# Kernel tuning notes

Hardware: AMD Instinct MI355X
Metric: run time of the kernel (lower is better)

## Reference

```python
import jax, jax.numpy as jnp
import numpy as np

NEG = -100.0
M2M, M2I, M2D, I2M, I2I, D2M, D2D = range(7)
LOG_Q = float(np.log(0.25))


def _d_chain(fM, aM2D, aD2D):
    """Sequential delete-state recurrence along motif axis k.
    fD[k] = logaddexp(aM2D[k-1] + fM[k-1], aD2D[k-1] + fD[k-1]), fD[0] = NEG.
    fM: (B, K+1); aM2D, aD2D: (B, K+1). Returns (B, K+1)."""
    B, Kp1 = fM.shape
    K = Kp1 - 1

    def step(fd_prev, inp):
        am, ad, fm = inp  # each (B,)
        fd = jnp.logaddexp(am + fm, ad + fd_prev)
        return fd, fd

    init = jnp.full((B,), NEG, dtype=fM.dtype)
    _, fds = jax.lax.scan(step, init, (aM2D[:, :K].T, aD2D[:, :K].T, fM[:, :K].T))
    return jnp.concatenate([init[:, None], fds.T], axis=1)


def _profile_hmm_loss(a, e, x):
    """pHMM forward algorithm (log-space). a: (B,K+1,7), e: (B,K,4), x: (B,L) int.
    Returns -log P(x) per batch element, shape (B,)."""
    B, Kp1, _ = a.shape
    K = Kp1 - 1

    fM0 = jnp.full((B, Kp1), NEG, dtype=a.dtype).at[:, 0].set(0.0)
    fI0 = jnp.full((B, Kp1), NEG, dtype=a.dtype)
    fD0 = _d_chain(fM0, a[:, :, M2D], a[:, :, D2D])

    def l_step(carry, x_l):
        fM, fI, fD = carry
        # emission for symbol x_l at each match state k: (B, K)
        esel = jnp.take_along_axis(e, x_l[:, None, None].astype(jnp.int32), axis=2)[:, :, 0]
        prev = jnp.logaddexp(
            jnp.logaddexp(a[:, :K, M2M] + fM[:, :K], a[:, :K, I2M] + fI[:, :K]),
            a[:, :K, D2M] + fD[:, :K],
        )
        fM_new = jnp.concatenate([jnp.full((B, 1), NEG, dtype=a.dtype), esel + prev], axis=1)
        fI_new = LOG_Q + jnp.logaddexp(a[:, :, M2I] + fM, a[:, :, I2I] + fI)
        fD_new = _d_chain(fM_new, a[:, :, M2D], a[:, :, D2D])
        return (fM_new, fI_new, fD_new), None

    (fM, fI, fD), _ = jax.lax.scan(l_step, (fM0, fI0, fD0), x.T)

    final = jnp.stack(
        [fM[:, K] + a[:, K, M2M], fI[:, K] + a[:, K, I2M], fD[:, K] + a[:, K, D2M]],
        axis=1,
    )
    return -jax.nn.logsumexp(final, axis=1)


def _kld_loss(mus, logvars):
    return -0.5 * jnp.sum(1.0 + logvars - mus * mus - jnp.exp(logvars), axis=1)


def setup_inputs() -> dict:
    key = jax.random.key(0)
    k1, k2, k3, k4, k5 = jax.random.split(key, 5)
    B, K, L, E = 4096, 64, 128, 16
    batch_input = jax.random.randint(k1, (B, L), 0, 4, dtype=jnp.int32)
    transition_probs = jax.random.normal(k2, (B, K + 1, 7), dtype=jnp.float32)
    emission_probs = jax.random.normal(k3, (B, K, 4), dtype=jnp.float32)
    mus = jax.random.normal(k4, (B, E), dtype=jnp.float32)
    logvars = jax.random.normal(k5, (B, E), dtype=jnp.float32)
    return {
        "batch_input": batch_input,
        "transition_probs": transition_probs,
        "emission_probs": emission_probs,
        "mus": mus,
        "logvars": logvars,
    }


def reference(batch_input, transition_probs, emission_probs, mus, logvars):
    beta = 1.0
    recon = jnp.mean(_profile_hmm_loss(transition_probs, emission_probs, batch_input))
    kld = jnp.mean(_kld_loss(mus, logvars))
    return recon + beta * kld
```

## Files before the change

### kernel.cpp

```cpp
#include <hip/hip_runtime.h>
#include <math.h>


namespace {

constexpr float kLog2e = 1.4426950408889634f;
constexpr float kLn2   = 0.6931471805599453f;

__device__ __forceinline__ float fexp(float x) {
    return __builtin_amdgcn_exp2f(x * kLog2e);
}

__device__ __forceinline__ float rflf(float x) {
    return __builtin_bit_cast(float,
        __builtin_amdgcn_readfirstlane(__builtin_bit_cast(int, x)));
}

template <int CTRL, bool BC>
__device__ __forceinline__ float dppf(float old, float src) {
    int r = __builtin_amdgcn_update_dpp(__builtin_bit_cast(int, old),
                                        __builtin_bit_cast(int, src),
                                        CTRL, 0xF, 0xF, BC);
    return __builtin_bit_cast(float, r);
}

__global__ __launch_bounds__(256) void phmm_vae_kernel(
    const int* __restrict__ xg,
    const float* __restrict__ ag,
    const float* __restrict__ eg,
    const float* __restrict__ mug,
    const float* __restrict__ lvg,
    float* __restrict__ out, int B)
{
    const int tid  = threadIdx.x;
    const int lane = tid & 63;
    const int wv   = tid >> 6;
    const int b    = (blockIdx.x << 2) + wv;

    __shared__ float part[4];
    float contrib = 0.0f;

    if (b < B) {
        const float* ab = ag + (size_t)b * 455;
        const float* eb = eg + (size_t)b * 256;
        const int*   xb = xg + (size_t)b * 128;

        const int j = lane;
        const float a2 = ab[j * 7 + 2];
        const float a6 = ab[j * 7 + 6];
        const float a5 = ab[(j + 1) * 7 + 5];
        const float A1M2M  = fexp(ab[(j + 1) * 7 + 0]);
        const float QA1M2I = 0.25f * fexp(ab[(j + 1) * 7 + 1]);
        const float A1I2M  = fexp(ab[(j + 1) * 7 + 3]);
        const float QA1I2I = 0.25f * fexp(ab[(j + 1) * 7 + 4]);
        const float A0M2M = fexp(ab[0]);
        const float D0f = rflf(0.25f * fexp(ab[4]));
        const float G0f = rflf(0.25f * fexp(ab[3] + ab[1] - ab[0]));

        float4 ev = *reinterpret_cast<const float4*>(eb + j * 4);
        const float E0 = fexp(ev.x), E1 = fexp(ev.y);
        const float E2 = fexp(ev.z), E3 = fexp(ev.w);

        const int xlo = xb[lane];
        const int xhi = xb[64 + lane];
        const unsigned long long b0lo = __ballot(xlo & 1);
        const unsigned long long b1lo = __ballot(xlo & 2);
        const unsigned long long b0hi = __ballot(xhi & 1);
        const unsigned long long b1hi = __ballot(xhi & 2);

        const float a5p = dppf<0x138, false>(0.0f, a5);
        const float dh  = fexp(a6 + a5 - a5p);
        const float wM2D = fexp(a2 + a5);
        const float Cf0 = wM2D * dppf<0x138, false>(0.0f, E0);
        const float Cf1 = wM2D * dppf<0x138, false>(0.0f, E1);
        const float Cf2 = wM2D * dppf<0x138, false>(0.0f, E2);
        const float Cf3 = wM2D * dppf<0x138, false>(0.0f, E3);

        auto bfr = [](float x) -> unsigned {
            unsigned u = __builtin_bit_cast(unsigned, x);
            return (u + 0x8000u) >> 16;
        };
        const int E10 = (int)((bfr(E1) << 16) | bfr(E0));
        const int E32 = (int)((bfr(E3) << 16) | bfr(E2));
        const int C10 = (int)((bfr(Cf1) << 16) | bfr(Cf0));
        const int C32 = (int)((bfr(Cf3) << 16) | bfr(Cf2));

        const float V1 = dh;
        const float V2 = V1 * dppf<0x111, false>(1.0f, V1);
        const float V4 = V2 * dppf<0x112, false>(1.0f, V2);
        const float V8 = V4 * dppf<0x114, false>(1.0f, V4);
        const float V1m = (lane >= 1)  ? V1 : 0.0f;
        const float V2m = (lane >= 2)  ? V2 : 0.0f;
        const float V4m = (lane >= 4)  ? V4 : 0.0f;
        const float V8m = (lane >= 8)  ? V8 : 0.0f;
        float Q = dh;
        Q *= dppf<0x111, false>(1.0f, Q);
        Q *= dppf<0x112, false>(1.0f, Q);
        Q *= dppf<0x114, false>(1.0f, Q);
        Q *= dppf<0x118, false>(1.0f, Q);
        const int   row = lane >> 4;
        const float Q47 = __shfl(Q, 47, 64);
        const float QmA = (row == 1 || row == 3) ? Q : 0.0f;
        const float QmB = (row == 2) ? Q : ((row == 3) ? Q * Q47 : 0.0f);

        float y0 = (lane == 0) ? wM2D : 0.0f;
        y0 = fmaf(V1m, dppf<0x111, true>(0.0f, y0), y0);
        y0 = fmaf(V2m, dppf<0x112, true>(0.0f, y0), y0);
        y0 = fmaf(V4m, dppf<0x114, true>(0.0f, y0), y0);
        y0 = fmaf(V8m, dppf<0x118, true>(0.0f, y0), y0);
        y0 = fmaf(QmA, dppf<0x142, true>(0.0f, y0), y0);
        y0 = fmaf(QmB, dppf<0x143, true>(0.0f, y0), y0);

        auto sel_of = [&](int l) -> int {
            const unsigned long long m0 = (l & 64) ? b0hi : b0lo;
            const unsigned long long m1 = (l & 64) ? b1hi : b1lo;
            const int sh = l & 63;
            unsigned s = (unsigned)((m0 >> sh) & 1ull) |
                         ((unsigned)((m1 >> sh) & 1ull) << 1);
            return (int)(0x00000C0Cu + s * 0x02020000u + 0x01000000u);
        };

        float fM = 0.0f, fI = 0.0f;
        float pl = y0;
        float p0 = A0M2M;
        float LS = 0.0f;

        const int sel0 = sel_of(0);
        float E = __builtin_bit_cast(float,
            __builtin_amdgcn_perm((unsigned)E32, (unsigned)E10, (unsigned)sel0));
        float C = __builtin_bit_cast(float,
            __builtin_amdgcn_perm((unsigned)C32, (unsigned)C10, (unsigned)sel0));

#pragma unroll 8
        for (int l = 0; l < 128; ++l) {
            const int seln = sel_of((l + 1) & 127);
            const float mul_s = (l == 0) ? G0f : D0f;

            float y, pv, En, Cn;
            asm("v_mul_f32 %[fI], %[QI2I], %[fI]\n\t"
                "v_mov_b32 %[pv], %[p0]\n\t"
                "v_perm_b32 %[En], %[e32], %[e10], %[sel]\n\t"
                "v_perm_b32 %[Cn], %[c32], %[c10], %[sel]\n\t"
                "v_mov_b32_dpp %[pv], %[pl] wave_shr:1 row_mask:0xf bank_mask:0xf\n\t"
                "v_fmac_f32 %[fI], %[QM2I], %[fM]\n\t"
                "v_mul_f32 %[p0], %[mul], %[p0]\n\t"
                "v_mul_f32_dpp %[y], %[pv], %[C] wave_shr:1 row_mask:0xf bank_mask:0xf bound_ctrl:0\n\t"
                "v_mul_f32 %[fM], %[E], %[pv]\n\t"
                "s_nop 0\n\t"
                "v_fmac_f32_dpp %[y], %[y], %[V1] row_shr:1 row_mask:0xf bank_mask:0xf bound_ctrl:0\n\t"
                "s_nop 1\n\t"
                "v_fmac_f32_dpp %[y], %[y], %[V2] row_shr:2 row_mask:0xf bank_mask:0xf bound_ctrl:0\n\t"
                "s_nop 1\n\t"
                "v_fmac_f32_dpp %[y], %[y], %[V4] row_shr:4 row_mask:0xf bank_mask:0xf bound_ctrl:0\n\t"
                "s_nop 1\n\t"
                "v_fmac_f32_dpp %[y], %[y], %[V8] row_shr:8 row_mask:0xf bank_mask:0xf bound_ctrl:0\n\t"
                "s_nop 1\n\t"
                "v_fmac_f32_dpp %[y], %[y], %[QmA] row_bcast:15 row_mask:0xf bank_mask:0xf bound_ctrl:0\n\t"
                "s_nop 1\n\t"
                "v_fmac_f32_dpp %[y], %[y], %[QmB] row_bcast:31 row_mask:0xf bank_mask:0xf bound_ctrl:0\n\t"
                "v_fmac_f32 %[y], %[I2M], %[fI]\n\t"
                "v_fmac_f32 %[y], %[M2M], %[fM]"
                : [y] "=&v"(y), [pv] "=&v"(pv), [En] "=&v"(En), [Cn] "=&v"(Cn),
                  [fM] "+v"(fM), [fI] "+v"(fI), [p0] "+v"(p0)
                : [pl] "v"(pl), [E] "v"(E), [C] "v"(C),
                  [e32] "v"(E32), [e10] "v"(E10),
                  [c32] "v"(C32), [c10] "v"(C10),
                  [V1] "v"(V1m), [V2] "v"(V2m), [V4] "v"(V4m), [V8] "v"(V8m),
                  [QmA] "v"(QmA), [QmB] "v"(QmB),
                  [QI2I] "v"(QA1I2I), [QM2I] "v"(QA1M2I),
                  [I2M] "v"(A1I2M), [M2M] "v"(A1M2M),
                  [sel] "s"(seln), [mul] "s"(mul_s));
            pl = y;
            E = En;
            C = Cn;

            if ((l & 15) == 15) {
                float m = fmaxf(fmaxf(fM, fI), pl);
                m = fmaxf(m, dppf<0xB1,  true>(0.0f, m));
                m = fmaxf(m, dppf<0x4E,  true>(0.0f, m));
                m = fmaxf(m, dppf<0x141, true>(0.0f, m));
                m = fmaxf(m, dppf<0x140, true>(0.0f, m));
                m = fmaxf(m, 1e-35f);
                int mb = __builtin_bit_cast(int, m);
                unsigned u0 = (unsigned)__builtin_amdgcn_readlane(mb, 0);
                unsigned u1 = (unsigned)__builtin_amdgcn_readlane(mb, 16);
                unsigned u2 = (unsigned)__builtin_amdgcn_readlane(mb, 32);
                unsigned u3 = (unsigned)__builtin_amdgcn_readlane(mb, 48);
                unsigned ua = u0 > u1 ? u0 : u1;
                unsigned ub = u2 > u3 ? u2 : u3;
                unsigned um = ua > ub ? ua : ub;
                int ee = (int)(um >> 23);
                float r = __builtin_bit_cast(float, (unsigned)(254 - ee) << 23);
                LS += (float)(ee - 127);
                fM *= r; fI *= r; pl *= r; p0 *= r;
            }
        }

        const float Fv = __shfl(pl, 63, 64);
        const float loss = -(__builtin_amdgcn_logf(Fv) + LS) * kLn2;

        float kt = 0.0f;
        if (lane < 16) {
            float mu = mug[(size_t)b * 16 + lane];
            float lv = lvg[(size_t)b * 16 + lane];
            kt = 1.0f + lv - mu * mu - fexp(lv);
        }
        kt += __shfl_xor(kt, 1, 64);
        kt += __shfl_xor(kt, 2, 64);
        kt += __shfl_xor(kt, 4, 64);
        kt += __shfl_xor(kt, 8, 64);
        float kldb = __shfl(-0.5f * kt, 0, 64);

        contrib = (loss + kldb) * (1.0f / 4096.0f);
    }

    if (lane == 63) part[wv] = (b < B) ? contrib : 0.0f;
    __syncthreads();
    if (tid == 0) {
        atomicAdd(out, part[0] + part[1] + part[2] + part[3]);
    }
}

}

extern "C" void kernel_launch(void* const* d_in, const int* in_sizes, int n_in,
                              void* d_out, int out_size, void* d_ws, size_t ws_size,
                              hipStream_t stream) {
    const int*   x  = (const int*)d_in[0];
    const float* a  = (const float*)d_in[1];
    const float* e  = (const float*)d_in[2];
    const float* mu = (const float*)d_in[3];
    const float* lv = (const float*)d_in[4];
    float* out = (float*)d_out;

    const int B = in_sizes[0] / 128;
    const int grid = (B + 3) / 4;

    phmm_vae_kernel<<<grid, 256, 0, stream>>>(x, a, e, mu, lv, out, B);
}
```

Before: 92.28 us.

## Process two batch elements per wave with interleaved DPP recurrence chains

Each wavefront now runs the forward recurrence for two sequences at once, interleaving their DPP scan instructions so each chain's dependent DPP ops fill the other's stall slots instead of explicit s_nop padding. The grid is halved accordingly, and the KLD term is computed for both elements using lanes 0-31. This roughly doubles per-wave register use and halves the number of waves, which may reduce latency hiding from occupancy; some inline-asm work moved to compiler-scheduled C++.

```diff
diff --git a/kernel.cpp b/kernel.cpp
--- a/kernel.cpp
+++ b/kernel.cpp
@@ -22,6 +22,125 @@
                                         __builtin_bit_cast(int, src),
                                         CTRL, 0xF, 0xF, BC);
     return __builtin_bit_cast(float, r);
+}
+
+__device__ __forceinline__ unsigned bfr(float x) {
+    unsigned u = __builtin_bit_cast(unsigned, x);
+    return (u + 0x8000u) >> 16;
+}
+
+struct Elem {
+    float fM, fI, pl, p0, E, C, LS;
+    float V1m, V2m, V4m, V8m, QmA, QmB;
+    float QI2I, QM2I, I2M, M2M;
+    float D0, G0;
+    int E10, E32, C10, C32;
+    unsigned long long b0lo, b1lo, b0hi, b1hi;
+};
+
+__device__ __forceinline__ int sel_of(const Elem& s, int l) {
+    const unsigned long long m0 = (l & 64) ? s.b0hi : s.b0lo;
+    const unsigned long long m1 = (l & 64) ? s.b1hi : s.b1lo;
+    const int sh = l & 63;
+    unsigned t = (unsigned)((m0 >> sh) & 1ull) |
+                 ((unsigned)((m1 >> sh) & 1ull) << 1);
+    return (int)(0x00000C0Cu + t * 0x02020000u + 0x01000000u);
+}
+
+__device__ __forceinline__ void setup(Elem& s, const float* __restrict__ ab,
+                                      const float* __restrict__ eb,
+                                      const int* __restrict__ xb, int lane) {
+    const int j = lane;
+    const float a2 = ab[j * 7 + 2];
+    const float a6 = ab[j * 7 + 6];
+    const float a5 = ab[(j + 1) * 7 + 5];
+    s.M2M  = fexp(ab[(j + 1) * 7 + 0]);
+    s.QM2I = 0.25f * fexp(ab[(j + 1) * 7 + 1]);
+    s.I2M  = fexp(ab[(j + 1) * 7 + 3]);
+    s.QI2I = 0.25f * fexp(ab[(j + 1) * 7 + 4]);
+    const float A0M2M = fexp(ab[0]);
+    s.D0 = rflf(0.25f * fexp(ab[4]));
+    s.G0 = rflf(0.25f * fexp(ab[3] + ab[1] - ab[0]));
+
+    float4 ev = *reinterpret_cast<const float4*>(eb + j * 4);
+    const float E0 = fexp(ev.x), E1 = fexp(ev.y);
+    const float E2 = fexp(ev.z), E3 = fexp(ev.w);
+
+    const int xlo = xb[lane];
+    const int xhi = xb[64 + lane];
+    s.b0lo = __ballot(xlo & 1);
+    s.b1lo = __ballot(xlo & 2);
+    s.b0hi = __ballot(xhi & 1);
+    s.b1hi = __ballot(xhi & 2);
+
+    const float a5p = dppf<0x138, false>(0.0f, a5);
+    const float dh  = fexp(a6 + a5 - a5p);
+    const float wM2D = fexp(a2 + a5);
+    const float Cf0 = wM2D * dppf<0x138, false>(0.0f, E0);
+    const float Cf1 = wM2D * dppf<0x138, false>(0.0f, E1);
+    const float Cf2 = wM2D * dppf<0x138, false>(0.0f, E2);
+    const float Cf3 = wM2D * dppf<0x138, false>(0.0f, E3);
+
+    s.E10 = (int)((bfr(E1) << 16) | bfr(E0));
+    s.E32 = (int)((bfr(E3) << 16) | bfr(E2));
+    s.C10 = (int)((bfr(Cf1) << 16) | bfr(Cf0));
+    s.C32 = (int)((bfr(Cf3) << 16) | bfr(Cf2));
+
+    const float V1 = dh;
+    const float V2 = V1 * dppf<0x111, false>(1.0f, V1);
+    const float V4 = V2 * dppf<0x112, false>(1.0f, V2);
+    const float V8 = V4 * dppf<0x114, false>(1.0f, V4);
+    s.V1m = (lane >= 1) ? V1 : 0.0f;
+    s.V2m = (lane >= 2) ? V2 : 0.0f;
+    s.V4m = (lane >= 4) ? V4 : 0.0f;
+    s.V8m = (lane >= 8) ? V8 : 0.0f;
+    float Q = dh;
+    Q *= dppf<0x111, false>(1.0f, Q);
+    Q *= dppf<0x112, false>(1.0f, Q);
+    Q *= dppf<0x114, false>(1.0f, Q);
+    Q *= dppf<0x118, false>(1.0f, Q);
+    const int   row = lane >> 4;
+    const float Q47 = __shfl(Q, 47, 64);
+    s.QmA = (row == 1 || row == 3) ? Q : 0.0f;
+    s.QmB = (row == 2) ? Q : ((row == 3) ? Q * Q47 : 0.0f);
+
+    float y0 = (lane == 0) ? wM2D : 0.0f;
+    y0 = fmaf(s.V1m, dppf<0x111, true>(0.0f, y0), y0);
+    y0 = fmaf(s.V2m, dppf<0x112, true>(0.0f, y0), y0);
+    y0 = fmaf(s.V4m, dppf<0x114, true>(0.0f, y0), y0);
+    y0 = fmaf(s.V8m, dppf<0x118, true>(0.0f, y0), y0);
+    y0 = fmaf(s.QmA, dppf<0x142, true>(0.0f, y0), y0);
+    y0 = fmaf(s.QmB, dppf<0x143, true>(0.0f, y0), y0);
+
+    s.fM = 0.0f; s.fI = 0.0f; s.LS = 0.0f;
+    s.pl = y0;
+    s.p0 = A0M2M;
+    const int sel0 = sel_of(s, 0);
+    s.E = __builtin_bit_cast(float,
+        __builtin_amdgcn_perm((unsigned)s.E32, (unsigned)s.E10, (unsigned)sel0));
+    s.C = __builtin_bit_cast(float,
+        __builtin_amdgcn_perm((unsigned)s.C32, (unsigned)s.C10, (unsigned)sel0));
+}
+
+__device__ __forceinline__ void rescale(Elem& s) {
+    float m = fmaxf(fmaxf(s.fM, s.fI), s.pl);
+    m = fmaxf(m, dppf<0xB1,  true>(0.0f, m));
+    m = fmaxf(m, dppf<0x4E,  true>(0.0f, m));
+    m = fmaxf(m, dppf<0x141, true>(0.0f, m));
+    m = fmaxf(m, dppf<0x140, true>(0.0f, m));
+    m = fmaxf(m, 1e-35f);
+    int mb = __builtin_bit_cast(int, m);
+    unsigned u0 = (unsigned)__builtin_amdgcn_readlane(mb, 0);
+    unsigned u1 = (unsigned)__builtin_amdgcn_readlane(mb, 16);
+    unsigned u2 = (unsigned)__builtin_amdgcn_readlane(mb, 32);
+    unsigned u3 = (unsigned)__builtin_amdgcn_readlane(mb, 48);
+    unsigned ua = u0 > u1 ? u0 : u1;
+    unsigned ub = u2 > u3 ? u2 : u3;
+    unsigned um = ua > ub ? ua : ub;
+    int ee = (int)(um >> 23);
+    float r = __builtin_bit_cast(float, (unsigned)(254 - ee) << 23);
+    s.LS += (float)(ee - 127);
+    s.fM *= r; s.fI *= r; s.pl *= r; s.p0 *= r;
 }
 
 __global__ __launch_bounds__(256) void phmm_vae_kernel(
@@ -35,186 +154,112 @@
     const int tid  = threadIdx.x;
     const int lane = tid & 63;
     const int wv   = tid >> 6;
-    const int b    = (blockIdx.x << 2) + wv;
+    const int pr   = (blockIdx.x << 2) + wv;
+    const int bA   = pr << 1;
+    const int bBr  = bA + 1;
 
     __shared__ float part[4];
     float contrib = 0.0f;
 
-    if (b < B) {
-        const float* ab = ag + (size_t)b * 455;
-        const float* eb = eg + (size_t)b * 256;
-        const int*   xb = xg + (size_t)b * 128;
-
-        const int j = lane;
-        const float a2 = ab[j * 7 + 2];
-        const float a6 = ab[j * 7 + 6];
-        const float a5 = ab[(j + 1) * 7 + 5];
-        const float A1M2M  = fexp(ab[(j + 1) * 7 + 0]);
-        const float QA1M2I = 0.25f * fexp(ab[(j + 1) * 7 + 1]);
-        const float A1I2M  = fexp(ab[(j + 1) * 7 + 3]);
-        const float QA1I2I = 0.25f * fexp(ab[(j + 1) * 7 + 4]);
-        const float A0M2M = fexp(ab[0]);
-        const float D0f = rflf(0.25f * fexp(ab[4]));
-        const float G0f = rflf(0.25f * fexp(ab[3] + ab[1] - ab[0]));
-
-        float4 ev = *reinterpret_cast<const float4*>(eb + j * 4);
-        const float E0 = fexp(ev.x), E1 = fexp(ev.y);
-        const float E2 = fexp(ev.z), E3 = fexp(ev.w);
-
-        const int xlo = xb[lane];
-        const int xhi = xb[64 + lane];
-        const unsigned long long b0lo = __ballot(xlo & 1);
-        const unsigned long long b1lo = __ballot(xlo & 2);
-        const unsigned long long b0hi = __ballot(xhi & 1);
-        const unsigned long long b1hi = __ballot(xhi & 2);
-
-        const float a5p = dppf<0x138, false>(0.0f, a5);
-        const float dh  = fexp(a6 + a5 - a5p);
-        const float wM2D = fexp(a2 + a5);
-        const float Cf0 = wM2D * dppf<0x138, false>(0.0f, E0);
-        const float Cf1 = wM2D * dppf<0x138, false>(0.0f, E1);
-        const float Cf2 = wM2D * dppf<0x138, false>(0.0f, E2);
-        const float Cf3 = wM2D * dppf<0x138, false>(0.0f, E3);
-
-        auto bfr = [](float x) -> unsigned {
-            unsigned u = __builtin_bit_cast(unsigned, x);
-            return (u + 0x8000u) >> 16;
-        };
-        const int E10 = (int)((bfr(E1) << 16) | bfr(E0));
-        const int E32 = (int)((bfr(E3) << 16) | bfr(E2));
-        const int C10 = (int)((bfr(Cf1) << 16) | bfr(Cf0));
-        const int C32 = (int)((bfr(Cf3) << 16) | bfr(Cf2));
-
-        const float V1 = dh;
-        const float V2 = V1 * dppf<0x111, false>(1.0f, V1);
-        const float V4 = V2 * dppf<0x112, false>(1.0f, V2);
-        const float V8 = V4 * dppf<0x114, false>(1.0f, V4);
-        const float V1m = (lane >= 1)  ? V1 : 0.0f;
-        const float V2m = (lane >= 2)  ? V2 : 0.0f;
-        const float V4m = (lane >= 4)  ? V4 : 0.0f;
-        const float V8m = (lane >= 8)  ? V8 : 0.0f;
-        float Q = dh;
-        Q *= dppf<0x111, false>(1.0f, Q);
-        Q *= dppf<0x112, false>(1.0f, Q);
-        Q *= dppf<0x114, false>(1.0f, Q);
-        Q *= dppf<0x118, false>(1.0f, Q);
-        const int   row = lane >> 4;
-        const float Q47 = __shfl(Q, 47, 64);
-        const float QmA = (row == 1 || row == 3) ? Q : 0.0f;
-        const float QmB = (row == 2) ? Q : ((row == 3) ? Q * Q47 : 0.0f);
-
-        float y0 = (lane == 0) ? wM2D : 0.0f;
-        y0 = fmaf(V1m, dppf<0x111, true>(0.0f, y0), y0);
-        y0 = fmaf(V2m, dppf<0x112, true>(0.0f, y0), y0);
-        y0 = fmaf(V4m, dppf<0x114, true>(0.0f, y0), y0);
-        y0 = fmaf(V8m, dppf<0x118, true>(0.0f, y0), y0);
-        y0 = fmaf(QmA, dppf<0x142, true>(0.0f, y0), y0);
-        y0 = fmaf(QmB, dppf<0x143, true>(0.0f, y0), y0);
-
-        auto sel_of = [&](int l) -> int {
-            const unsigned long long m0 = (l & 64) ? b0hi : b0lo;
-            const unsigned long long m1 = (l & 64) ? b1hi : b1lo;
-            const int sh = l & 63;
-            unsigned s = (unsigned)((m0 >> sh) & 1ull) |
-                         ((unsigned)((m1 >> sh) & 1ull) << 1);
-            return (int)(0x00000C0Cu + s * 0x02020000u + 0x01000000u);
-        };
-
-        float fM = 0.0f, fI = 0.0f;
-        float pl = y0;
-        float p0 = A0M2M;
-        float LS = 0.0f;
-
-        const int sel0 = sel_of(0);
-        float E = __builtin_bit_cast(float,
-            __builtin_amdgcn_perm((unsigned)E32, (unsigned)E10, (unsigned)sel0));
-        float C = __builtin_bit_cast(float,
-            __builtin_amdgcn_perm((unsigned)C32, (unsigned)C10, (unsigned)sel0));
+    if (bA < B) {
+        const bool hasB = (bBr < B);
+        const int  bB   = hasB ? bBr : bA;
+
+        Elem A, Bs;
+        setup(A,  ag + (size_t)bA * 455, eg + (size_t)bA * 256,
+              xg + (size_t)bA * 128, lane);
+        setup(Bs, ag + (size_t)bB * 455, eg + (size_t)bB * 256,
+              xg + (size_t)bB * 128, lane);
 
 #pragma unroll 8
         for (int l = 0; l < 128; ++l) {
-            const int seln = sel_of((l + 1) & 127);
-            const float mul_s = (l == 0) ? G0f : D0f;
-
-            float y, pv, En, Cn;
-            asm("v_mul_f32 %[fI], %[QI2I], %[fI]\n\t"
-                "v_mov_b32 %[pv], %[p0]\n\t"
-                "v_perm_b32 %[En], %[e32], %[e10], %[sel]\n\t"
-                "v_perm_b32 %[Cn], %[c32], %[c10], %[sel]\n\t"
-                "v_mov_b32_dpp %[pv], %[pl] wave_shr:1 row_mask:0xf bank_mask:0xf\n\t"
-                "v_fmac_f32 %[fI], %[QM2I], %[fM]\n\t"
-                "v_mul_f32 %[p0], %[mul], %[p0]\n\t"
-                "v_mul_f32_dpp %[y], %[pv], %[C] wave_shr:1 row_mask:0xf bank_mask:0xf bound_ctrl:0\n\t"
-                "v_mul_f32 %[fM], %[E], %[pv]\n\t"
-                "s_nop 0\n\t"
-                "v_fmac_f32_dpp %[y], %[y], %[V1] row_shr:1 row_mask:0xf bank_mask:0xf bound_ctrl:0\n\t"
-                "s_nop 1\n\t"
-                "v_fmac_f32_dpp %[y], %[y], %[V2] row_shr:2 row_mask:0xf bank_mask:0xf bound_ctrl:0\n\t"
-                "s_nop 1\n\t"
-                "v_fmac_f32_dpp %[y], %[y], %[V4] row_shr:4 row_mask:0xf bank_mask:0xf bound_ctrl:0\n\t"
-                "s_nop 1\n\t"
-                "v_fmac_f32_dpp %[y], %[y], %[V8] row_shr:8 row_mask:0xf bank_mask:0xf bound_ctrl:0\n\t"
-                "s_nop 1\n\t"
-                "v_fmac_f32_dpp %[y], %[y], %[QmA] row_bcast:15 row_mask:0xf bank_mask:0xf bound_ctrl:0\n\t"
-                "s_nop 1\n\t"
-                "v_fmac_f32_dpp %[y], %[y], %[QmB] row_bcast:31 row_mask:0xf bank_mask:0xf bound_ctrl:0\n\t"
-                "v_fmac_f32 %[y], %[I2M], %[fI]\n\t"
-                "v_fmac_f32 %[y], %[M2M], %[fM]"
-                : [y] "=&v"(y), [pv] "=&v"(pv), [En] "=&v"(En), [Cn] "=&v"(Cn),
-                  [fM] "+v"(fM), [fI] "+v"(fI), [p0] "+v"(p0)
-                : [pl] "v"(pl), [E] "v"(E), [C] "v"(C),
-                  [e32] "v"(E32), [e10] "v"(E10),
-                  [c32] "v"(C32), [c10] "v"(C10),
-                  [V1] "v"(V1m), [V2] "v"(V2m), [V4] "v"(V4m), [V8] "v"(V8m),
-                  [QmA] "v"(QmA), [QmB] "v"(QmB),
-                  [QI2I] "v"(QA1I2I), [QM2I] "v"(QA1M2I),
-                  [I2M] "v"(A1I2M), [M2M] "v"(A1M2M),
-                  [sel] "s"(seln), [mul] "s"(mul_s));
-            pl = y;
-            E = En;
-            C = Cn;
-
-            if ((l & 15) == 15) {
-                float m = fmaxf(fmaxf(fM, fI), pl);
-                m = fmaxf(m, dppf<0xB1,  true>(0.0f, m));
-                m = fmaxf(m, dppf<0x4E,  true>(0.0f, m));
-                m = fmaxf(m, dppf<0x141, true>(0.0f, m));
-                m = fmaxf(m, dppf<0x140, true>(0.0f, m));
-                m = fmaxf(m, 1e-35f);
-                int mb = __builtin_bit_cast(int, m);
-                unsigned u0 = (unsigned)__builtin_amdgcn_readlane(mb, 0);
-                unsigned u1 = (unsigned)__builtin_amdgcn_readlane(mb, 16);
-                unsigned u2 = (unsigned)__builtin_amdgcn_readlane(mb, 32);
-                unsigned u3 = (unsigned)__builtin_amdgcn_readlane(mb, 48);
-                unsigned ua = u0 > u1 ? u0 : u1;
-                unsigned ub = u2 > u3 ? u2 : u3;
-                unsigned um = ua > ub ? ua : ub;
-                int ee = (int)(um >> 23);
-                float r = __builtin_bit_cast(float, (unsigned)(254 - ee) << 23);
-                LS += (float)(ee - 127);
-                fM *= r; fI *= r; pl *= r; p0 *= r;
-            }
+            const int selA = sel_of(A,  (l + 1) & 127);
+            const int selB = sel_of(Bs, (l + 1) & 127);
+            const float mulA = (l == 0) ? A.G0  : A.D0;
+            const float mulB = (l == 0) ? Bs.G0 : Bs.D0;
+
+            A.fI  = fmaf(A.QM2I,  A.fM,  A.QI2I  * A.fI);
+            Bs.fI = fmaf(Bs.QM2I, Bs.fM, Bs.QI2I * Bs.fI);
+
+            float yA, yB, pvA, pvB, fMA, fMB;
+            asm("v_mov_b32 %[pvA], %[p0A]\n\t"
+                "v_mov_b32 %[pvB], %[p0B]\n\t"
+                "v_mov_b32_dpp %[pvA], %[plA] wave_shr:1 row_mask:0xf bank_mask:0xf\n\t"
+                "v_mov_b32_dpp %[pvB], %[plB] wave_shr:1 row_mask:0xf bank_mask:0xf\n\t"
+                "v_mul_f32_dpp %[yA], %[pvA], %[CA] wave_shr:1 row_mask:0xf bank_mask:0xf bound_ctrl:0\n\t"
+                "v_mul_f32_dpp %[yB], %[pvB], %[CB] wave_shr:1 row_mask:0xf bank_mask:0xf bound_ctrl:0\n\t"
+                "v_mul_f32 %[fMA], %[EA], %[pvA]\n\t"
+                "v_mul_f32 %[fMB], %[EB], %[pvB]\n\t"
+                "v_fmac_f32_dpp %[yA], %[yA], %[V1A] row_shr:1 row_mask:0xf bank_mask:0xf bound_ctrl:0\n\t"
+                "v_fmac_f32_dpp %[yB], %[yB], %[V1B] row_shr:1 row_mask:0xf bank_mask:0xf bound_ctrl:0\n\t"
+                "v_fmac_f32_dpp %[yA], %[yA], %[V2A] row_shr:2 row_mask:0xf bank_mask:0xf bound_ctrl:0\n\t"
+                "v_fmac_f32_dpp %[yB], %[yB], %[V2B] row_shr:2 row_mask:0xf bank_mask:0xf bound_ctrl:0\n\t"
+                "v_fmac_f32_dpp %[yA], %[yA], %[V4A] row_shr:4 row_mask:0xf bank_mask:0xf bound_ctrl:0\n\t"
+                "v_fmac_f32_dpp %[yB], %[yB], %[V4B] row_shr:4 row_mask:0xf bank_mask:0xf bound_ctrl:0\n\t"
+                "v_fmac_f32_dpp %[yA], %[yA], %[V8A] row_shr:8 row_mask:0xf bank_mask:0xf bound_ctrl:0\n\t"
+                "v_fmac_f32_dpp %[yB], %[yB], %[V8B] row_shr:8 row_mask:0xf bank_mask:0xf bound_ctrl:0\n\t"
+                "v_fmac_f32_dpp %[yA], %[yA], %[QmAA] row_bcast:15 row_mask:0xf bank_mask:0xf bound_ctrl:0\n\t"
+                "v_fmac_f32_dpp %[yB], %[yB], %[QmAB] row_bcast:15 row_mask:0xf bank_mask:0xf bound_ctrl:0\n\t"
+                "v_fmac_f32_dpp %[yA], %[yA], %[QmBA] row_bcast:31 row_mask:0xf bank_mask:0xf bound_ctrl:0\n\t"
+                "v_fmac_f32_dpp %[yB], %[yB], %[QmBB] row_bcast:31 row_mask:0xf bank_mask:0xf bound_ctrl:0"
+                : [yA] "=&v"(yA), [yB] "=&v"(yB),
+                  [pvA] "=&v"(pvA), [pvB] "=&v"(pvB),
+                  [fMA] "=&v"(fMA), [fMB] "=&v"(fMB)
+                : [plA] "v"(A.pl), [plB] "v"(Bs.pl),
+                  [p0A] "v"(A.p0), [p0B] "v"(Bs.p0),
+                  [CA] "v"(A.C), [CB] "v"(Bs.C),
+                  [EA] "v"(A.E), [EB] "v"(Bs.E),
+                  [V1A] "v"(A.V1m), [V2A] "v"(A.V2m),
+                  [V4A] "v"(A.V4m), [V8A] "v"(A.V8m),
+                  [QmAA] "v"(A.QmA), [QmBA] "v"(A.QmB),
+                  [V1B] "v"(Bs.V1m), [V2B] "v"(Bs.V2m),
+                  [V4B] "v"(Bs.V4m), [V8B] "v"(Bs.V8m),
+                  [QmAB] "v"(Bs.QmA), [QmBB] "v"(Bs.QmB));
+
+            A.fM = fMA;  Bs.fM = fMB;
+            A.p0 *= mulA;  Bs.p0 *= mulB;
+            A.pl  = fmaf(A.M2M,  fMA, fmaf(A.I2M,  A.fI,  yA));
+            Bs.pl = fmaf(Bs.M2M, fMB, fmaf(Bs.I2M, Bs.fI, yB));
+            A.E  = __builtin_bit_cast(float, __builtin_amdgcn_perm(
+                       (unsigned)A.E32,  (unsigned)A.E10,  (unsigned)selA));
+            A.C  = __builtin_bit_cast(float, __builtin_amdgcn_perm(
+                       (unsigned)A.C32,  (unsigned)A.C10,  (unsigned)selA));
+            Bs.E = __builtin_bit_cast(float, __builtin_amdgcn_perm(
+                       (unsigned)Bs.E32, (unsigned)Bs.E10, (unsigned)selB));
+            Bs.C = __builtin_bit_cast(float, __builtin_amdgcn_perm(
+                       (unsigned)Bs.C32, (unsigned)Bs.C10, (unsigned)selB));
+
+            if ((l & 15) == 15) { rescale(A); rescale(Bs); }
         }
 
-        const float Fv = __shfl(pl, 63, 64);
-        const float loss = -(__builtin_amdgcn_logf(Fv) + LS) * kLn2;
+        const float FvA = __shfl(A.pl,  63, 64);
+        const float FvB = __shfl(Bs.pl, 63, 64);
+        const float lossA = -(__builtin_amdgcn_logf(FvA) + A.LS)  * kLn2;
+        const float lossB = -(__builtin_amdgcn_logf(FvB) + Bs.LS) * kLn2;
 
         float kt = 0.0f;
         if (lane < 16) {
-            float mu = mug[(size_t)b * 16 + lane];
-            float lv = lvg[(size_t)b * 16 + lane];
+            float mu = mug[(size_t)bA * 16 + lane];
+            float lv = lvg[(size_t)bA * 16 + lane];
+            kt = 1.0f + lv - mu * mu - fexp(lv);
+        } else if (lane < 32) {
+            const int ln = lane - 16;
+            float mu = mug[(size_t)bB * 16 + ln];
+            float lv = lvg[(size_t)bB * 16 + ln];
             kt = 1.0f + lv - mu * mu - fexp(lv);
         }
         kt += __shfl_xor(kt, 1, 64);
         kt += __shfl_xor(kt, 2, 64);
         kt += __shfl_xor(kt, 4, 64);
         kt += __shfl_xor(kt, 8, 64);
-        float kldb = __shfl(-0.5f * kt, 0, 64);
-
-        contrib = (loss + kldb) * (1.0f / 4096.0f);
+        const float kldA = -0.5f * __shfl(kt, 0, 64);
+        const float kldB = -0.5f * __shfl(kt, 16, 64);
+
+        contrib = (lossA + kldA + (hasB ? (lossB + kldB) : 0.0f))
+                  * (1.0f / 4096.0f);
     }
 
-    if (lane == 63) part[wv] = (b < B) ? contrib : 0.0f;
+    if (lane == 63) part[wv] = (bA < B) ? contrib : 0.0f;
     __syncthreads();
     if (tid == 0) {
         atomicAdd(out, part[0] + part[1] + part[2] + part[3]);
@@ -234,7 +279,8 @@
     float* out = (float*)d_out;
 
     const int B = in_sizes[0] / 128;
-    const int grid = (B + 3) / 4;
+    const int npairs = (B + 1) >> 1;
+    const int grid = (npairs + 3) / 4;
 
     phmm_vae_kernel<<<grid, 256, 0, stream>>>(x, a, e, mu, lv, out, B);
 }
```

Measured after the change: 92.97 us. No clear change (+0.7%).
